# Kernel optimization log

Hardware: AMD Instinct MI355X
Metric: run time of the kernel (lower is better)

Reference implementation:

```python
import jax, jax.numpy as jnp
import numpy as np

HIDDEN = 2048
NUM_HEADS = 16
HEAD_DIM = HIDDEN // NUM_HEADS


def setup_inputs() -> dict:
    key = jax.random.key(0)
    k1, k2, k3 = jax.random.split(key, 3)
    B, S = 2, 2048
    hidden_states = jax.random.normal(k1, (B, S, HIDDEN), dtype=jnp.float32)
    attention_mask = jnp.zeros((B, 1, 1, S), dtype=jnp.float32)
    W_qkv = jax.random.normal(k2, (HIDDEN, 3 * HIDDEN), dtype=jnp.float32) * (1.0 / np.sqrt(HIDDEN))
    b_qkv = jnp.zeros((3 * HIDDEN,), dtype=jnp.float32)
    W_out = jax.random.normal(k3, (HIDDEN, HIDDEN), dtype=jnp.float32) * (1.0 / np.sqrt(HIDDEN))
    b_out = jnp.zeros((HIDDEN,), dtype=jnp.float32)
    return {"hidden_states": hidden_states, "attention_mask": attention_mask,
            "W_qkv": W_qkv, "b_qkv": b_qkv, "W_out": W_out, "b_out": b_out}


def reference(hidden_states, attention_mask, W_qkv, b_qkv, W_out, b_out):
    B, S, H = hidden_states.shape
    scale = 1.0 / np.sqrt(HEAD_DIM)
    # fused QKV projection (column-parallel linear, world_size=1)
    mixed = hidden_states @ W_qkv + b_qkv                      # [B,S,3H]
    q, k, v = jnp.split(mixed, 3, axis=-1)
    # [B, heads, S, head_dim]
    q = q.reshape(B, S, NUM_HEADS, HEAD_DIM).transpose(0, 2, 1, 3)
    k = k.reshape(B, S, NUM_HEADS, HEAD_DIM).transpose(0, 2, 1, 3)
    v = v.reshape(B, S, NUM_HEADS, HEAD_DIM).transpose(0, 2, 1, 3)
    scores = jnp.einsum('bhqd,bhkd->bhqk', q, k) * scale       # [B,h,S,S]
    scores = scores + attention_mask                            # additive mask broadcast
    probs = jax.nn.softmax(scores, axis=-1)
    ctx = jnp.einsum('bhqk,bhkd->bhqd', probs, v)               # [B,h,S,d]
    ctx = ctx.transpose(0, 2, 1, 3).reshape(B, S, H)
    return ctx @ W_out + b_out
```

## Files before the change

kernel.cpp:

```cpp
#include <hip/hip_runtime.h>
#include <hip/hip_bf16.h>
#include <stdint.h>

typedef __attribute__((ext_vector_type(4))) float   f32x4;
typedef __attribute__((ext_vector_type(8))) __bf16  bf16x8;
typedef __attribute__((ext_vector_type(4))) __bf16  bf16x4;
typedef __attribute__((ext_vector_type(8))) short   s16x8;
typedef __attribute__((ext_vector_type(4))) unsigned short u16x4;
typedef __attribute__((ext_vector_type(4))) float   fl4;

#define DEVFN static __device__ __forceinline__

constexpr int BATCH = 2, SEQ = 2048, HID = 2048, NHEAD = 16, HDIM = 128;
constexpr int MROWS = BATCH * SEQ;
constexpr int N3    = 3 * HID;
constexpr float ATT_SCALE = 0.08838834764831845f;
constexpr float LOG2E = 1.44269504088896340736f;

DEVFN unsigned short f2bf(float f) {
  unsigned int u = __float_as_uint(f);
  u += 0x7FFFu + ((u >> 16) & 1u);
  return (unsigned short)(u >> 16);
}
DEVFN float bf2f(unsigned short h) { return __uint_as_float(((unsigned int)h) << 16); }

DEVFN void async_cp16(const void* g, void* l) {
  __builtin_amdgcn_global_load_lds(
      (__attribute__((address_space(1))) void*)g,
      (__attribute__((address_space(3))) void*)l, 16, 0, 0);
}

DEVFN f32x4 mfma_bf16(bf16x8 a, bf16x8 b, f32x4 c) {
  return __builtin_amdgcn_mfma_f32_16x16x32_bf16(a, b, c, 0, 0, 0);
}

__global__ __launch_bounds__(256) void cvt_bf16(const float* __restrict__ x,
                                                unsigned short* __restrict__ hi, int n4) {
  for (int i = blockIdx.x * blockDim.x + threadIdx.x; i < n4; i += gridDim.x * blockDim.x) {
    fl4 v = ((const fl4*)x)[i];
    u16x4 h;
#pragma unroll
    for (int j = 0; j < 4; j++) h[j] = f2bf(v[j]);
    ((u16x4*)hi)[i] = h;
  }
}

__global__ __launch_bounds__(256) void cvt_transpose(const float* __restrict__ W,
                                                     unsigned short* __restrict__ T,
                                                     int R, int C) {
  __shared__ float tile[32][33];
  const int c0 = blockIdx.x * 32, r0 = blockIdx.y * 32;
  const int tx = threadIdx.x, ty = threadIdx.y;
#pragma unroll
  for (int i = 0; i < 4; i++) tile[ty + 8 * i][tx] = W[(size_t)(r0 + ty + 8 * i) * C + c0 + tx];
  __syncthreads();
#pragma unroll
  for (int i = 0; i < 4; i++) {
    const float v = tile[tx][ty + 8 * i];
    T[(size_t)(c0 + ty + 8 * i) * R + r0 + tx] = f2bf(v);
  }
}

template <bool OUT_BF16>
__global__ __launch_bounds__(512, 1) void gemm_ring(const unsigned short* __restrict__ A,
                                                    const unsigned short* __restrict__ Bt,
                                                    const float* __restrict__ bias,
                                                    void* __restrict__ Cout, int Ndim) {
  constexpr int KDIM  = 2048;
  constexpr int NT    = KDIM / 64;
  constexpr int ASLOT = 256 * 64;
  constexpr int BSLOT = 128 * 64;
  constexpr int SLOT  = ASLOT + BSLOT;
  __shared__ __align__(16) unsigned short smem[3 * SLOT];

  const int tid = threadIdx.x;
  const int wid = tid >> 6, lane = tid & 63;
  const int wm = wid >> 2, wn = wid & 3;
  const int g = lane >> 4, q = lane & 15;
  const int n0 = blockIdx.x * 128, m0 = blockIdx.y * 256;

  const int srow = (wid << 3) + (lane >> 3);
  const int scol = (((lane & 7) ^ (lane >> 3)) << 4);
  const char* gA = (const char*)A  + ((size_t)(m0 + srow) * KDIM) * 2 + scol;
  const char* gB = (const char*)Bt + ((size_t)(n0 + srow) * KDIM) * 2 + scol;
  const int dbase = ((wid << 3)) << 7;

  f32x4 acc[8][2] = {};
  const int axor = (q & 7) << 4;

  auto STAGE = [&](int tt, int slot) {
    char* sA = (char*)(smem + slot * SLOT);
    char* sB = (char*)(smem + slot * SLOT + ASLOT);
    const size_t koff = (size_t)tt << 7;
#pragma unroll
    for (int i = 0; i < 4; i++)
      async_cp16(gA + (size_t)(i * 64) * (KDIM * 2) + koff, sA + dbase + (i << 13));
#pragma unroll
    for (int i = 0; i < 2; i++)
      async_cp16(gB + (size_t)(i * 64) * (KDIM * 2) + koff, sB + dbase + (i << 13));
  };

  auto COMPUTE = [&](int slot) {
    const char* sA = (const char*)(smem + slot * SLOT);
    const char* sB = (const char*)(smem + slot * SLOT + ASLOT);
#pragma unroll
    for (int ks = 0; ks < 2; ks++) {
      const int kb = (ks << 6) + (g << 4);
      bf16x8 av[8], bv[2];
#pragma unroll
      for (int nf = 0; nf < 2; nf++) {
        const int row = (wn << 5) + (nf << 4) + q;
        bv[nf] = *(const bf16x8*)(sB + (row << 7) + (kb ^ axor));
      }
#pragma unroll
      for (int mf = 0; mf < 8; mf++) {
        const int row = (wm << 7) + (mf << 4) + q;
        av[mf] = *(const bf16x8*)(sA + (row << 7) + (kb ^ axor));
      }
#pragma unroll
      for (int mf = 0; mf < 8; mf++)
#pragma unroll
        for (int nf = 0; nf < 2; nf++)
          acc[mf][nf] = mfma_bf16(av[mf], bv[nf], acc[mf][nf]);
    }
  };

  STAGE(0, 0);
  STAGE(1, 1);
  int s2 = 2, sc = 0;
#pragma unroll 1
  for (int t = 0; t < NT - 2; ++t) {
    asm volatile("s_waitcnt vmcnt(6)" ::: "memory");
    __builtin_amdgcn_s_barrier();
    asm volatile("" ::: "memory");
    STAGE(t + 2, s2);
    COMPUTE(sc);
    s2 = (s2 == 2) ? 0 : s2 + 1;
    sc = (sc == 2) ? 0 : sc + 1;
  }
  asm volatile("s_waitcnt vmcnt(6)" ::: "memory");
  __builtin_amdgcn_s_barrier();
  asm volatile("" ::: "memory");
  COMPUTE(sc);
  sc = (sc == 2) ? 0 : sc + 1;
  asm volatile("s_waitcnt vmcnt(0)" ::: "memory");
  __builtin_amdgcn_s_barrier();
  asm volatile("" ::: "memory");
  COMPUTE(sc);

  float bvv[2];
#pragma unroll
  for (int nf = 0; nf < 2; nf++) bvv[nf] = bias[n0 + (wn << 5) + (nf << 4) + q];
#pragma unroll
  for (int mf = 0; mf < 8; mf++) {
    const int rowg = m0 + (wm << 7) + (mf << 4) + (g << 2);
#pragma unroll
    for (int nf = 0; nf < 2; nf++) {
      const int colg = n0 + (wn << 5) + (nf << 4) + q;
#pragma unroll
      for (int r = 0; r < 4; r++) {
        const float v = acc[mf][nf][r] + bvv[nf];
        if (OUT_BF16)
          ((unsigned short*)Cout)[(size_t)(rowg + r) * Ndim + colg] = f2bf(v);
        else
          ((float*)Cout)[(size_t)(rowg + r) * Ndim + colg] = v;
      }
    }
  }
}

__global__ __launch_bounds__(256) void transpose_v(const unsigned short* __restrict__ qkv,
                                                   unsigned short* __restrict__ vt) {
  __shared__ __align__(16) unsigned short tile[64][136];
  const int z = blockIdx.y, b = z >> 4, h = z & 15;
  const int s0 = blockIdx.x << 6;
  const int t = threadIdx.x;
#pragma unroll
  for (int i = 0; i < 4; i++) {
    const int idx = t + (i << 8);
    const int row = idx >> 4, ch = idx & 15;
    *(s16x8*)&tile[row][ch << 3] =
        *(const s16x8*)(qkv + (size_t)(b * SEQ + s0 + row) * N3 + 2 * HID + h * HDIM + (ch << 3));
  }
  __syncthreads();
#pragma unroll
  for (int i = 0; i < 4; i++) {
    const int idx = t + (i << 8);
    const int d = idx >> 3, sc = idx & 7;
    s16x8 v;
#pragma unroll
    for (int j = 0; j < 8; j++) v[j] = (short)tile[(sc << 3) + j][d];
    *(s16x8*)(vt + (size_t)(z * HDIM + d) * SEQ + s0 + (sc << 3)) = v;
  }
}

__global__ __launch_bounds__(256, 2) void attn_kernel(const unsigned short* __restrict__ qkv,
                                                      const unsigned short* __restrict__ vt,
                                                      const float* __restrict__ mask,
                                                      unsigned short* __restrict__ ctx) {
  __shared__ __align__(16) unsigned short sK[64 * 128];
  __shared__ __align__(16) unsigned short sV[128 * 64];
  __shared__ __align__(16) unsigned short sP[4][32 * 72];

  const int z = blockIdx.y, b = z >> 4, h = z & 15;
  const int qb = blockIdx.x;
  const int tid = threadIdx.x, wid = tid >> 6, lane = tid & 63;
  const int g = lane >> 4, q = lane & 15;
  const int q0 = (qb << 7) + (wid << 5);

  bf16x8 bq[2][4];
#pragma unroll
  for (int qs = 0; qs < 2; qs++) {
    const unsigned short* qrow = qkv + (size_t)(b * SEQ + q0 + (qs << 4) + q) * N3 + h * HDIM;
#pragma unroll
    for (int c = 0; c < 4; c++) bq[qs][c] = *(const bf16x8*)(qrow + (c << 5) + (g << 3));
  }

  f32x4 acc[2][8] = {};
  float mrun[2] = {-1e30f, -1e30f}, lrun[2] = {0.f, 0.f};
  const int lrow8 = lane >> 3, lcol8 = (lane & 7) << 4;
  const int lrow16 = lane >> 4, lcol16 = (lane & 15) << 4;
  unsigned short* myP = &sP[wid][0];
  const int sbase = (lane & 48) | (g << 2);

  for (int k0 = 0; k0 < SEQ; k0 += 64) {
    __syncthreads();
#pragma unroll
    for (int i = 0; i < 4; i++) {
      const int kr = (wid << 4) + (i << 2) + lrow16;
      const int kcol = lcol16 ^ ((kr & 7) << 4);
      async_cp16((const char*)qkv + (((size_t)(b * SEQ + k0 + kr) * N3 + HID + h * HDIM) << 1) + kcol,
                 (char*)sK + (((wid << 4) + (i << 2)) << 8));
      const int vr = (wid << 5) + (i << 3) + lrow8;
      const int vcol = lcol8 ^ ((vr & 7) << 4);
      async_cp16((const char*)vt + (((size_t)(z * HDIM + vr) * SEQ + k0) << 1) + vcol,
                 (char*)sV + (((wid << 5) + (i << 3)) << 7));
    }
    __syncthreads();

    f32x4 accs[2][4];
#pragma unroll
    for (int qs = 0; qs < 2; qs++)
#pragma unroll
      for (int kt = 0; kt < 4; kt++) accs[qs][kt] = (f32x4){0.f, 0.f, 0.f, 0.f};
#pragma unroll
    for (int c = 0; c < 4; c++) {
      const int kbyte = (c << 6) + (g << 4);
#pragma unroll
      for (int kt = 0; kt < 4; kt++) {
        const int key = (kt << 4) + q;
        const bf16x8 ak = *(const bf16x8*)((const char*)sK + (key << 8) + (kbyte ^ ((key & 7) << 4)));
        accs[0][kt] = mfma_bf16(ak, bq[0][c], accs[0][kt]);
        accs[1][kt] = mfma_bf16(ak, bq[1][c], accs[1][kt]);
      }
    }

#pragma unroll
    for (int qs = 0; qs < 2; qs++) {
      float sv[4][4];
      float mt = -1e30f;
#pragma unroll
      for (int kt = 0; kt < 4; kt++) {
        const fl4 mk = *(const fl4*)(mask + (size_t)b * SEQ + k0 + (kt << 4) + (g << 2));
#pragma unroll
        for (int r = 0; r < 4; r++) {
          const float s = accs[qs][kt][r] * ATT_SCALE + mk[r];
          sv[kt][r] = s;
          mt = fmaxf(mt, s);
        }
      }
      mt = fmaxf(mt, __shfl_xor(mt, 16));
      mt = fmaxf(mt, __shfl_xor(mt, 32));
      if (!__all(mt <= mrun[qs] + 8.f)) {
        const float mnew = fmaxf(mrun[qs], mt);
        const float fs = exp2f((mrun[qs] - mnew) * LOG2E);
        lrun[qs] *= fs;
#pragma unroll
        for (int r = 0; r < 4; r++) {
          const float fr = __shfl(fs, sbase + r);
#pragma unroll
          for (int dt = 0; dt < 8; dt++) acc[qs][dt][r] *= fr;
        }
        mrun[qs] = mnew;
      }
      float ps = 0.f;
#pragma unroll
      for (int kt = 0; kt < 4; kt++) {
        bf16x4 pk;
#pragma unroll
        for (int r = 0; r < 4; r++) {
          const float e = exp2f((sv[kt][r] - mrun[qs]) * LOG2E);
          ps += e;
          pk[r] = (__bf16)e;
        }
        *(bf16x4*)((char*)myP + ((qs << 4) + q) * 144 + (((kt << 4) + (g << 2)) << 1)) = pk;
      }
      ps += __shfl_xor(ps, 16);
      ps += __shfl_xor(ps, 32);
      lrun[qs] += ps;
    }

    asm volatile("s_waitcnt lgkmcnt(0)" ::: "memory");
    __builtin_amdgcn_sched_barrier(0);

#pragma unroll
    for (int kc = 0; kc < 2; kc++) {
      const bf16x8 pa0 = *(const bf16x8*)((const char*)myP + q * 144 + (kc << 6) + (g << 4));
      const bf16x8 pa1 = *(const bf16x8*)((const char*)myP + (16 + q) * 144 + (kc << 6) + (g << 4));
      const int kbyte = (kc << 6) + (g << 4);
#pragma unroll
      for (int dt = 0; dt < 8; dt++) {
        const int d = (dt << 4) + q;
        const bf16x8 bvv = *(const bf16x8*)((const char*)sV + (d << 7) + (kbyte ^ ((d & 7) << 4)));
        acc[0][dt] = mfma_bf16(pa0, bvv, acc[0][dt]);
        acc[1][dt] = mfma_bf16(pa1, bvv, acc[1][dt]);
      }
    }
  }

#pragma unroll
  for (int qs = 0; qs < 2; qs++)
#pragma unroll
    for (int r = 0; r < 4; r++) {
      const float lr = __shfl(lrun[qs], sbase + r);
      const float inv = 1.f / lr;
      const int token = b * SEQ + (qb << 7) + (wid << 5) + (qs << 4) + (g << 2) + r;
      unsigned short* crow = ctx + (size_t)token * HID + h * HDIM + q;
#pragma unroll
      for (int dt = 0; dt < 8; dt++) crow[dt << 4] = f2bf(acc[qs][dt][r] * inv);
    }
}

extern "C" void kernel_launch(void* const* d_in, const int* in_sizes, int n_in,
                              void* d_out, int out_size, void* d_ws, size_t ws_size,
                              hipStream_t stream) {
  const float* hs   = (const float*)d_in[0];
  const float* mask = (const float*)d_in[1];
  const float* Wqkv = (const float*)d_in[2];
  const float* bqkv = (const float*)d_in[3];
  const float* Wout = (const float*)d_in[4];
  const float* bout = (const float*)d_in[5];

  char* ws = (char*)d_ws;
  size_t off = 0;
  auto alloc = [&](size_t n) { char* p = ws + off; off += (n + 255) & ~(size_t)255; return p; };
  unsigned short* hs_bf = (unsigned short*)alloc((size_t)MROWS * HID * 2);
  unsigned short* wq_bf = (unsigned short*)alloc((size_t)N3 * HID * 2);
  unsigned short* wo_bf = (unsigned short*)alloc((size_t)HID * HID * 2);
  unsigned short* qkvb  = (unsigned short*)alloc((size_t)MROWS * N3 * 2);
  unsigned short* vtb   = (unsigned short*)alloc((size_t)BATCH * NHEAD * HDIM * SEQ * 2);
  unsigned short* ctxb  = (unsigned short*)alloc((size_t)MROWS * HID * 2);
  (void)ws_size;

  cvt_bf16<<<2048, 256, 0, stream>>>(hs, hs_bf, MROWS * HID / 4);
  dim3 tb(32, 8);
  cvt_transpose<<<dim3(N3 / 32, HID / 32), tb, 0, stream>>>(Wqkv, wq_bf, HID, N3);
  cvt_transpose<<<dim3(HID / 32, HID / 32), tb, 0, stream>>>(Wout, wo_bf, HID, HID);
  gemm_ring<true ><<<dim3(N3 / 128, MROWS / 256), 512, 0, stream>>>(hs_bf, wq_bf, bqkv, qkvb, N3);
  transpose_v<<<dim3(SEQ / 64, BATCH * NHEAD), 256, 0, stream>>>(qkvb, vtb);
  attn_kernel<<<dim3(SEQ / 128, BATCH * NHEAD), 256, 0, stream>>>(qkvb, vtb, mask, ctxb);
  gemm_ring<false><<<dim3(HID / 128, MROWS / 256), 512, 0, stream>>>(ctxb, wo_bf, bout, (float*)d_out, HID);
}
```

Before: 278.0 us.

## Triple-buffer K/V tiles in attention with 8-wave blocks and remapped grid

After: 277.5 us. Within noise of the previous version (-0.2%).

```diff
diff --git a/kernel.cpp b/kernel.cpp
--- a/kernel.cpp
+++ b/kernel.cpp
@@ -194,19 +194,24 @@
   }
 }
 
-__global__ __launch_bounds__(256, 2) void attn_kernel(const unsigned short* __restrict__ qkv,
+__global__ __launch_bounds__(512, 2) void attn_kernel(const unsigned short* __restrict__ qkv,
                                                       const unsigned short* __restrict__ vt,
                                                       const float* __restrict__ mask,
                                                       unsigned short* __restrict__ ctx) {
-  __shared__ __align__(16) unsigned short sK[64 * 128];
-  __shared__ __align__(16) unsigned short sV[128 * 64];
-  __shared__ __align__(16) unsigned short sP[4][32 * 72];
-
-  const int z = blockIdx.y, b = z >> 4, h = z & 15;
-  const int qb = blockIdx.x;
+  constexpr int NT    = SEQ / 64;
+  constexpr int KSLOT = 64 * 128;
+  constexpr int VSLOT = 128 * 64;
+  constexpr int SLOT  = KSLOT + VSLOT;
+  __shared__ __align__(16) unsigned short sKV[3 * SLOT];
+  __shared__ __align__(16) unsigned short sP[8][32 * 72];
+
+  const int bid = blockIdx.x;
+  const int z  = ((bid & 7) << 2) + ((bid >> 3) >> 3);
+  const int qb = (bid >> 3) & 7;
+  const int b = z >> 4, h = z & 15;
   const int tid = threadIdx.x, wid = tid >> 6, lane = tid & 63;
   const int g = lane >> 4, q = lane & 15;
-  const int q0 = (qb << 7) + (wid << 5);
+  const int q0 = (qb << 8) + (wid << 5);
 
   bf16x8 bq[2][4];
 #pragma unroll
@@ -218,25 +223,34 @@
 
   f32x4 acc[2][8] = {};
   float mrun[2] = {-1e30f, -1e30f}, lrun[2] = {0.f, 0.f};
-  const int lrow8 = lane >> 3, lcol8 = (lane & 7) << 4;
-  const int lrow16 = lane >> 4, lcol16 = (lane & 15) << 4;
   unsigned short* myP = &sP[wid][0];
   const int sbase = (lane & 48) | (g << 2);
 
-  for (int k0 = 0; k0 < SEQ; k0 += 64) {
-    __syncthreads();
-#pragma unroll
-    for (int i = 0; i < 4; i++) {
-      const int kr = (wid << 4) + (i << 2) + lrow16;
-      const int kcol = lcol16 ^ ((kr & 7) << 4);
-      async_cp16((const char*)qkv + (((size_t)(b * SEQ + k0 + kr) * N3 + HID + h * HDIM) << 1) + kcol,
-                 (char*)sK + (((wid << 4) + (i << 2)) << 8));
-      const int vr = (wid << 5) + (i << 3) + lrow8;
-      const int vcol = lcol8 ^ ((vr & 7) << 4);
-      async_cp16((const char*)vt + (((size_t)(z * HDIM + vr) * SEQ + k0) << 1) + vcol,
-                 (char*)sV + (((wid << 5) + (i << 3)) << 7));
-    }
-    __syncthreads();
+  const char* gK = (const char*)qkv + ((size_t)(b * SEQ) * N3 + HID + h * HDIM) * 2;
+  const char* gV = (const char*)vt + ((size_t)z * HDIM * SEQ) * 2;
+
+  auto STAGE = [&](int tt, int slot) {
+    char* base = (char*)(sKV + slot * SLOT);
+    const int k0 = tt << 6;
+#pragma unroll
+    for (int i = 0; i < 2; i++) {
+      const int krow = (i << 5) + (tid >> 4);
+      const int kc = (((tid & 15) << 4)) ^ ((krow & 7) << 4);
+      async_cp16(gK + ((size_t)(k0 + krow) * N3) * 2 + kc, base + (i << 13) + (wid << 10));
+    }
+#pragma unroll
+    for (int i = 0; i < 2; i++) {
+      const int vrow = (i << 6) + (tid >> 3);
+      const int vc = (((tid & 7) << 4)) ^ ((vrow & 7) << 4);
+      async_cp16(gV + ((size_t)vrow * SEQ + k0) * 2 + vc,
+                 base + (KSLOT * 2) + (i << 13) + (wid << 10));
+    }
+  };
+
+  auto COMPUTE = [&](int t, int slot) {
+    const char* sK = (const char*)(sKV + slot * SLOT);
+    const char* sV = (const char*)(sKV + slot * SLOT + KSLOT);
+    const int k0 = t << 6;
 
     f32x4 accs[2][4];
 #pragma unroll
@@ -249,7 +263,7 @@
 #pragma unroll
       for (int kt = 0; kt < 4; kt++) {
         const int key = (kt << 4) + q;
-        const bf16x8 ak = *(const bf16x8*)((const char*)sK + (key << 8) + (kbyte ^ ((key & 7) << 4)));
+        const bf16x8 ak = *(const bf16x8*)(sK + (key << 8) + (kbyte ^ ((key & 7) << 4)));
         accs[0][kt] = mfma_bf16(ak, bq[0][c], accs[0][kt]);
         accs[1][kt] = mfma_bf16(ak, bq[1][c], accs[1][kt]);
       }
@@ -311,12 +325,35 @@
 #pragma unroll
       for (int dt = 0; dt < 8; dt++) {
         const int d = (dt << 4) + q;
-        const bf16x8 bvv = *(const bf16x8*)((const char*)sV + (d << 7) + (kbyte ^ ((d & 7) << 4)));
+        const bf16x8 bvv = *(const bf16x8*)(sV + (d << 7) + (kbyte ^ ((d & 7) << 4)));
         acc[0][dt] = mfma_bf16(pa0, bvv, acc[0][dt]);
         acc[1][dt] = mfma_bf16(pa1, bvv, acc[1][dt]);
       }
     }
-  }
+  };
+
+  STAGE(0, 0);
+  STAGE(1, 1);
+  int s2 = 2, sc = 0;
+#pragma unroll 1
+  for (int t = 0; t < NT - 2; ++t) {
+    asm volatile("s_waitcnt vmcnt(4)" ::: "memory");
+    __builtin_amdgcn_s_barrier();
+    asm volatile("" ::: "memory");
+    STAGE(t + 2, s2);
+    COMPUTE(t, sc);
+    s2 = (s2 == 2) ? 0 : s2 + 1;
+    sc = (sc == 2) ? 0 : sc + 1;
+  }
+  asm volatile("s_waitcnt vmcnt(4)" ::: "memory");
+  __builtin_amdgcn_s_barrier();
+  asm volatile("" ::: "memory");
+  COMPUTE(NT - 2, sc);
+  sc = (sc == 2) ? 0 : sc + 1;
+  asm volatile("s_waitcnt vmcnt(0)" ::: "memory");
+  __builtin_amdgcn_s_barrier();
+  asm volatile("" ::: "memory");
+  COMPUTE(NT - 1, sc);
 
 #pragma unroll
   for (int qs = 0; qs < 2; qs++)
@@ -324,7 +361,7 @@
     for (int r = 0; r < 4; r++) {
       const float lr = __shfl(lrun[qs], sbase + r);
       const float inv = 1.f / lr;
-      const int token = b * SEQ + (qb << 7) + (wid << 5) + (qs << 4) + (g << 2) + r;
+      const int token = b * SEQ + q0 + (qs << 4) + (g << 2) + r;
       unsigned short* crow = ctx + (size_t)token * HID + h * HDIM + q;
 #pragma unroll
       for (int dt = 0; dt < 8; dt++) crow[dt << 4] = f2bf(acc[qs][dt][r] * inv);
@@ -358,6 +395,6 @@
   cvt_transpose<<<dim3(HID / 32, HID / 32), tb, 0, stream>>>(Wout, wo_bf, HID, HID);
   gemm_ring<true ><<<dim3(N3 / 128, MROWS / 256), 512, 0, stream>>>(hs_bf, wq_bf, bqkv, qkvb, N3);
   transpose_v<<<dim3(SEQ / 64, BATCH * NHEAD), 256, 0, stream>>>(qkvb, vtb);
-  attn_kernel<<<dim3(SEQ / 128, BATCH * NHEAD), 256, 0, stream>>>(qkvb, vtb, mask, ctxb);
+  attn_kernel<<<256, 512, 0, stream>>>(qkvb, vtb, mask, ctxb);
   gemm_ring<false><<<dim3(HID / 128, MROWS / 256), 512, 0, stream>>>(ctxb, wo_bf, bout, (float*)d_out, HID);
 }
```
